# Kernel optimization log

Measured on AMD Instinct MI355X. Metric: run time of the kernel, lower is better.

Reference implementation:

```python
import jax, jax.numpy as jnp
import numpy as np

B, T, C = 4, 2048, 1024
NH = 16
HD = C // NH  # 64

def setup_inputs() -> dict:
    key = jax.random.key(0)
    k1, k2, k3 = jax.random.split(key, 3)
    x = jax.random.normal(k1, (B, T, C), dtype=jnp.float32)
    w_qkv = jax.random.normal(k2, (C, 3 * C), dtype=jnp.float32) * (1.0 / np.sqrt(C))
    w_out = jax.random.normal(k3, (C, C), dtype=jnp.float32) * (1.0 / np.sqrt(C))
    b_out = jnp.zeros((C,), dtype=jnp.float32)
    return {"x": x, "w_qkv": w_qkv, "w_out": w_out, "b_out": b_out}

def reference(x, w_qkv, w_out, b_out):
    b, t, c = x.shape
    nh, hd = NH, c // NH
    qkv = x @ w_qkv                      # [b, t, 3c]
    q, k, v = jnp.split(qkv, 3, axis=-1)
    # [b, t, c] -> [b, nh, t, hd]
    def heads(z):
        return z.reshape(b, t, nh, hd).transpose(0, 2, 1, 3)
    q, k, v = heads(q), heads(k), heads(v)
    scale = 1.0 / jnp.sqrt(jnp.asarray(hd, dtype=x.dtype))
    scores = jnp.einsum('bhqd,bhkd->bhqk', q, k) * scale  # [b, nh, t, t]
    causal = jnp.tril(jnp.ones((t, t), dtype=bool))
    scores = jnp.where(causal, scores, jnp.asarray(-jnp.inf, dtype=scores.dtype))
    attn = jax.nn.softmax(scores, axis=-1)
    ctx = jnp.einsum('bhqk,bhkd->bhqd', attn, v)           # [b, nh, t, hd]
    ctx = ctx.transpose(0, 2, 1, 3).reshape(b, t, c)
    return ctx @ w_out + b_out
```

## Files before the change

### kernel.cpp

```cpp
#include <hip/hip_runtime.h>
#include <cmath>


typedef __bf16 bf16x4 __attribute__((ext_vector_type(4)));
typedef __bf16 bf16x8 __attribute__((ext_vector_type(8)));
typedef float  f32x4  __attribute__((ext_vector_type(4)));
typedef float  f32x16 __attribute__((ext_vector_type(16)));

__device__ __forceinline__ void gload_lds16(const __bf16* g, __bf16* l) {
    __builtin_amdgcn_global_load_lds(
        (const __attribute__((address_space(1))) void*)g,
        (__attribute__((address_space(3))) void*)l,
        16, 0, 0);
}

__device__ __forceinline__ unsigned packbf(float a, float b) {
    union { __bf16 h[2]; unsigned u; } t;
    t.h[0] = (__bf16)a; t.h[1] = (__bf16)b;
    return t.u;
}

__device__ __forceinline__ void permswap(unsigned& a, unsigned& b) {
    asm volatile("v_permlane32_swap_b32 %0, %1" : "+v"(a), "+v"(b));
}

#define BAR()  __builtin_amdgcn_s_barrier()
#define VM2()  { asm volatile("s_waitcnt vmcnt(2)" ::: "memory"); \
                 __builtin_amdgcn_sched_barrier(0); }

__global__ __launch_bounds__(256) void cast_bf16(const float* __restrict__ in,
                                                 __bf16* __restrict__ out, int n4) {
    int i = blockIdx.x * 256 + threadIdx.x;
    if (i >= n4) return;
    float4 f = *(const float4*)(in + (size_t)i * 4);
    bf16x4 o;
    o[0] = (__bf16)f.x; o[1] = (__bf16)f.y; o[2] = (__bf16)f.z; o[3] = (__bf16)f.w;
    *(bf16x4*)(out + (size_t)i * 4) = o;
}

__global__ __launch_bounds__(256) void transpose_cast(const float* __restrict__ W,
                                                      __bf16* __restrict__ WT,
                                                      int K, int N,
                                                      int nScaleLim, float scale) {
    __shared__ float tile[32][33];
    const int n0 = blockIdx.x * 32, k0 = blockIdx.y * 32;
    const int tx = threadIdx.x & 31, ty = threadIdx.x >> 5;
    #pragma unroll
    for (int i = 0; i < 4; ++i)
        tile[ty + 8 * i][tx] = W[(size_t)(k0 + ty + 8 * i) * N + n0 + tx];
    __syncthreads();
    #pragma unroll
    for (int i = 0; i < 4; ++i) {
        const int n = n0 + ty + 8 * i;
        float v = tile[tx][ty + 8 * i];
        if (n < nScaleLim) v *= scale;
        WT[(size_t)n * K + k0 + tx] = (__bf16)v;
    }
}

template <typename OutT, bool BIAS, bool VOUT>
__global__ __launch_bounds__(512) void gemm256(const __bf16* __restrict__ A,
                                               const __bf16* __restrict__ BT,
                                               OutT* __restrict__ Cc,
                                               const float* __restrict__ bias,
                                               __bf16* __restrict__ Vt,
                                               int M, int N, int K) {
    __shared__ __attribute__((aligned(16))) char lds[98304];
    const int tid = threadIdx.x, lane = tid & 63, w = tid >> 6;
    const int wr = w >> 1, wc = w & 1, cc = lane & 15, gg = lane >> 4;

    const int cpx = gridDim.x >> 3;
    const int swz = ((int)blockIdx.x & 7) * cpx + ((int)blockIdx.x >> 3);
    const int nbx = N >> 7;
    const int rowBase = (swz / nbx) << 8;
    const int colBase = (swz % nbx) << 7;
    const int NT = K >> 6;

    const int sChunk = (lane & 7) ^ (((lane >> 5) & 1) << 1);
    const int rsub   = lane >> 3;

    auto stA = [&](int t, int h) {
        const int buf = t & 1, k0 = (t % NT) * 64;
        #pragma unroll
        for (int l = 0; l < 2; ++l) {
            int idx   = l * 8 + w;
            int rbase = h * 128 + idx * 8;
            gload_lds16(A + (size_t)(rowBase + rbase + rsub) * K + k0 + sChunk * 8,
                        (__bf16*)(lds + buf * 32768 + rbase * 128 + lane * 16));
        }
    };
    auto stB = [&](int t) {
        const int buf = t & 1, k0 = (t % NT) * 64;
        #pragma unroll
        for (int l = 0; l < 2; ++l) {
            int idx   = l * 8 + w;
            int rbase = idx * 8;
            gload_lds16(BT + (size_t)(colBase + rbase + rsub) * K + k0 + sChunk * 8,
                        (__bf16*)(lds + 65536 + buf * 16384 + rbase * 128 + lane * 16));
        }
    };

    f32x4 acc[4][4];
    #pragma unroll
    for (int i = 0; i < 4; ++i)
        #pragma unroll
        for (int j = 0; j < 4; ++j) acc[i][j] = f32x4{0.f, 0.f, 0.f, 0.f};
    bf16x8 afr[4], bfr[8];

    auto rdA = [&](int buf, int mh) {
        const char* base = lds + buf * 32768;
        #pragma unroll
        for (int i = 0; i < 2; ++i)
            #pragma unroll
            for (int kk = 0; kk < 2; ++kk) {
                int r  = wr * 64 + mh * 32 + i * 16 + cc;
                int cb = (kk * 64 + gg * 16) ^ (((cc >> 2) & 1) << 5);
                afr[i * 2 + kk] = *(const bf16x8*)(base + r * 128 + cb);
            }
    };
    auto rdB = [&](int buf) {
        const char* base = lds + 65536 + buf * 16384;
        #pragma unroll
        for (int j = 0; j < 4; ++j)
            #pragma unroll
            for (int kk = 0; kk < 2; ++kk) {
                int r  = wc * 64 + j * 16 + cc;
                int cb = (kk * 64 + gg * 16) ^ (((cc >> 2) & 1) << 5);
                bfr[j * 2 + kk] = *(const bf16x8*)(base + r * 128 + cb);
            }
    };

#define QMFMA(MH, NH)                                                        \
    _Pragma("unroll") for (int i = 0; i < 2; ++i)                            \
    _Pragma("unroll") for (int j = 0; j < 2; ++j)                            \
    _Pragma("unroll") for (int kk = 0; kk < 2; ++kk)                         \
        acc[(MH)*2 + i][(NH)*2 + j] = __builtin_amdgcn_mfma_f32_16x16x32_bf16( \
            afr[i*2 + kk], bfr[((NH)*2 + j)*2 + kk], acc[(MH)*2 + i][(NH)*2 + j], 0, 0, 0);

    stA(0, 0); stB(0); stA(0, 1); stB(1);
    VM2(); BAR();

    for (int t = 0; t < NT; ++t) {
        const int buf = t & 1;
        rdA(buf, 0); rdB(buf);
        stA(t + 1, 0);
        BAR();
        __builtin_amdgcn_s_setprio(1); QMFMA(0, 0); __builtin_amdgcn_s_setprio(0);
        BAR();
        stA(t + 1, 1);
        BAR();
        __builtin_amdgcn_s_setprio(1); QMFMA(0, 1); __builtin_amdgcn_s_setprio(0);
        BAR();
        rdA(buf, 1);
        stB(t + 2);
        BAR();
        __builtin_amdgcn_s_setprio(1); QMFMA(1, 0); __builtin_amdgcn_s_setprio(0);
        BAR();
        BAR();
        __builtin_amdgcn_s_setprio(1); QMFMA(1, 1); __builtin_amdgcn_s_setprio(0);
        VM2(); BAR();
    }
#undef QMFMA

    #pragma unroll
    for (int i = 0; i < 4; ++i)
        #pragma unroll
        for (int j = 0; j < 4; ++j) {
            const int col = colBase + wc * 64 + j * 16 + cc;
            #pragma unroll
            for (int rr = 0; rr < 4; ++rr) {
                const int row = rowBase + wr * 64 + i * 16 + gg * 4 + rr;
                float v = acc[i][j][rr];
                if (BIAS) v += bias[col];
                Cc[(size_t)row * N + col] = (OutT)v;
            }
            if (VOUT && col >= 2048) {
                const int bh16 = ((rowBase >> 11) << 4) + ((col - 2048) >> 6);
                const int d    = (col - 2048) & 63;
                const int t0   = (rowBase & 2047) + wr * 64 + i * 16 + gg * 4;
                union { bf16x4 v4; uint2 u; } pk;
                #pragma unroll
                for (int rr = 0; rr < 4; ++rr) pk.v4[rr] = (__bf16)acc[i][j][rr];
                *(uint2*)(Vt + ((size_t)bh16 * 64 + d) * 2048 + t0) = pk.u;
            }
        }
}

__global__ __launch_bounds__(256) void flash_attn_mfma(const __bf16* __restrict__ qkv,
                                                       const __bf16* __restrict__ Vt,
                                                       __bf16* __restrict__ ctx) {
    constexpr int T = 2048, C = 1024, HD = 64;
    constexpr int R3C = 3 * C;

    const int tid  = threadIdx.x;
    const int lane = tid & 63;
    const int w    = tid >> 6;
    const int q5   = lane & 31;
    const int half = lane >> 5;

    const int bh   = blockIdx.x;
    const int y    = blockIdx.y;
    const int qtA  = 15 - y;
    const int qtB  = y;
    const int b    = bh >> 4;
    const int h    = bh & 15;
    const int srowA = qtA * 128 + w * 32;
    const int srowB = qtB * 128 + w * 32;
    const int ktmaxA = qtA * 128 + 64;
    const int ktmaxB = qtB * 128 + 64;

    __shared__ __attribute__((aligned(16))) __bf16 KsL[2][64][64];
    __shared__ __attribute__((aligned(16))) __bf16 VsL[2][64][64];

    const __bf16* QrowA = qkv + (size_t)(b * T + srowA + q5) * R3C + h * HD;
    const __bf16* QrowB = qkv + (size_t)(b * T + srowB + q5) * R3C + h * HD;
    bf16x8 QbA[4], QbB[4];
    #pragma unroll
    for (int ks = 0; ks < 4; ++ks) {
        QbA[ks] = *(const bf16x8*)(QrowA + ks * 16 + half * 8);
        QbB[ks] = *(const bf16x8*)(QrowB + ks * 16 + half * 8);
    }

    f32x16 OA[2], OB[2];
    #pragma unroll
    for (int mb = 0; mb < 2; ++mb)
        #pragma unroll
        for (int r = 0; r < 16; ++r) { OA[mb][r] = 0.f; OB[mb][r] = 0.f; }
    float lsumA = 0.f, lsumB = 0.f;

    const __bf16* Kb  = qkv + (size_t)(b * T) * R3C + C + h * HD;
    const __bf16* Vtb = Vt + (size_t)bh * 64 * T;

    auto stage = [&](int bufi, int kt) {
        #pragma unroll
        for (int i = 0; i < 2; ++i) {
            int idx = tid + 256 * i;
            int kr  = idx >> 3;
            int c8  = idx & 7;
            int cs  = c8 ^ (kr & 7);
            gload_lds16(Kb + (size_t)(kt + kr) * R3C + cs * 8,
                        &KsL[bufi][kr][c8 * 8]);
        }
        #pragma unroll
        for (int i = 0; i < 2; ++i) {
            int idx = tid + 256 * i;
            int d   = idx >> 3;
            int k8  = idx & 7;
            int ks_ = k8 ^ (d & 7);
            gload_lds16(Vtb + (size_t)d * T + kt + ks_ * 8,
                        &VsL[bufi][d][k8 * 8]);
        }
    };

    stage(0, 0);
    __syncthreads();

    for (int kt = 0; kt <= ktmaxA; kt += 64) {
        const int cur = (kt >> 6) & 1;
        if (kt + 64 <= ktmaxA) stage(cur ^ 1, kt + 64);

        const char* kbase = (const char*)KsL[cur];
        const char* vbase = (const char*)VsL[cur];

        auto subtile = [&](int sub, const bf16x8* Qb, int srow, f32x16* O, float& lsum) {
            f32x16 S;
            #pragma unroll
            for (int r = 0; r < 16; ++r) S[r] = 0.f;
            const int krow = sub * 32 + q5;
            const int kxor = (krow & 7) << 4;
            #pragma unroll
            for (int ks = 0; ks < 4; ++ks) {
                bf16x8 kb = *(const bf16x8*)(kbase + krow * 128 +
                                             (((ks * 16 + half * 8) * 2) ^ kxor));
                S = __builtin_amdgcn_mfma_f32_32x32x16_bf16(kb, Qb[ks], S, 0, 0, 0);
            }
            if (kt + sub * 32 + 31 > srow) {
                #pragma unroll
                for (int r = 0; r < 16; ++r) {
                    int key = kt + sub * 32 + (r & 3) + 8 * (r >> 2) + 4 * half;
                    if (key > srow + q5) S[r] = -1e30f;
                }
            }
            float p[16];
            #pragma unroll
            for (int r = 0; r < 16; ++r) p[r] = exp2f(S[r]);
            {
                float a0 = (p[0] + p[1]) + (p[2] + p[3]);
                float a1 = (p[4] + p[5]) + (p[6] + p[7]);
                float a2 = (p[8] + p[9]) + (p[10] + p[11]);
                float a3 = (p[12] + p[13]) + (p[14] + p[15]);
                lsum += (a0 + a1) + (a2 + a3);
            }
            unsigned w0 = packbf(p[0],  p[1]);
            unsigned w1 = packbf(p[2],  p[3]);
            unsigned w2 = packbf(p[4],  p[5]);
            unsigned w3 = packbf(p[6],  p[7]);
            permswap(w0, w2);
            permswap(w1, w3);
            unsigned w4 = packbf(p[8],  p[9]);
            unsigned w5 = packbf(p[10], p[11]);
            unsigned w6 = packbf(p[12], p[13]);
            unsigned w7 = packbf(p[14], p[15]);
            permswap(w4, w6);
            permswap(w5, w7);
            union { unsigned u[4]; bf16x8 v; } pf0, pf1;
            pf0.u[0] = w0; pf0.u[1] = w1; pf0.u[2] = w2; pf0.u[3] = w3;
            pf1.u[0] = w4; pf1.u[1] = w5; pf1.u[2] = w6; pf1.u[3] = w7;
            const int vc = sub * 32 + half * 8;
            #pragma unroll
            for (int mb = 0; mb < 2; ++mb) {
                const int vrow = mb * 32 + q5;
                const int vxor = (vrow & 7) << 4;
                bf16x8 v0 = *(const bf16x8*)(vbase + vrow * 128 + ((vc * 2) ^ vxor));
                O[mb] = __builtin_amdgcn_mfma_f32_32x32x16_bf16(v0, pf0.v, O[mb], 0, 0, 0);
                bf16x8 v1 = *(const bf16x8*)(vbase + vrow * 128 + (((vc + 16) * 2) ^ vxor));
                O[mb] = __builtin_amdgcn_mfma_f32_32x32x16_bf16(v1, pf1.v, O[mb], 0, 0, 0);
            }
        };

        #pragma unroll
        for (int sub = 0; sub < 2; ++sub)
            subtile(sub, QbA, srowA, OA, lsumA);
        if (kt <= ktmaxB) {
            #pragma unroll
            for (int sub = 0; sub < 2; ++sub)
                subtile(sub, QbB, srowB, OB, lsumB);
        }

        __syncthreads();
    }

    const float invA = 1.f / (lsumA + __shfl_xor(lsumA, 32));
    const float invB = 1.f / (lsumB + __shfl_xor(lsumB, 32));

    __bf16* crowA = ctx + (size_t)(b * T + srowA + q5) * C + h * HD;
    __bf16* crowB = ctx + (size_t)(b * T + srowB + q5) * C + h * HD;
    #pragma unroll
    for (int mb = 0; mb < 2; ++mb)
        #pragma unroll
        for (int a = 0; a < 4; ++a) {
            union { bf16x4 v; uint2 u; } pA, pB;
            #pragma unroll
            for (int bq = 0; bq < 4; ++bq) {
                pA.v[bq] = (__bf16)(OA[mb][4 * a + bq] * invA);
                pB.v[bq] = (__bf16)(OB[mb][4 * a + bq] * invB);
            }
            *(uint2*)(crowA + mb * 32 + 8 * a + 4 * half) = pA.u;
            *(uint2*)(crowB + mb * 32 + 8 * a + 4 * half) = pB.u;
        }
}

extern "C" void kernel_launch(void* const* d_in, const int* in_sizes, int n_in,
                              void* d_out, int out_size, void* d_ws, size_t ws_size,
                              hipStream_t stream) {
    constexpr int B = 4, T = 2048, C = 1024;
    constexpr int M = B * T;
    constexpr float K1 = 0.125f * 1.44269504088896f;

    const float* x     = (const float*)d_in[0];
    const float* w_qkv = (const float*)d_in[1];
    const float* w_out = (const float*)d_in[2];
    const float* b_out = (const float*)d_in[3];
    float* out = (float*)d_out;

    char* ws = (char*)d_ws;
    __bf16* xb     = (__bf16*)(ws);
    __bf16* wqkvT  = (__bf16*)(ws + (16ull << 20));
    __bf16* woutT  = (__bf16*)(ws + (22ull << 20));
    __bf16* qkvb   = (__bf16*)(ws + (24ull << 20));
    __bf16* ctxb   = (__bf16*)(ws + (72ull << 20));
    __bf16* Vt     = (__bf16*)(ws + (88ull << 20));

    cast_bf16<<<(M * C / 4 + 255) / 256, 256, 0, stream>>>(x, xb, M * C / 4);
    transpose_cast<<<dim3(3 * C / 32, C / 32), 256, 0, stream>>>(
        w_qkv, wqkvT, C, 3 * C, 1024, K1);
    transpose_cast<<<dim3(C / 32, C / 32), 256, 0, stream>>>(
        w_out, woutT, C, C, 0, 1.0f);

    gemm256<__bf16, false, true><<<768, 512, 0, stream>>>(
        xb, wqkvT, qkvb, nullptr, Vt, M, 3 * C, C);

    flash_attn_mfma<<<dim3(B * 16, 8), 256, 0, stream>>>(qkvb, Vt, ctxb);

    gemm256<float, true, false><<<256, 512, 0, stream>>>(
        ctxb, woutT, out, b_out, nullptr, M, C, C);
}
```

Baseline: 273.4 us.

## Split paired causal query tiles into separate blocks with interleaved tile order

Each flash-attention block used to handle two query tiles (a long and a short one) so causal work was balanced and K/V tiles were shared between them. Now each block handles one query tile, the grid doubles to 16 tiles per head, and tiles are mapped in an interleaved order so long and short tiles are mixed across blocks. This lowers per-block registers (one accumulator set instead of two), which may raise occupancy, and gives more blocks to spread over CUs. The cost is that K/V tiles are loaded twice as often and per-block work becomes uneven again.

```diff
diff --git a/kernel.cpp b/kernel.cpp
--- a/kernel.cpp
+++ b/kernel.cpp
@@ -198,35 +198,33 @@
     const int q5   = lane & 31;
     const int half = lane >> 5;
 
-    const int bh   = blockIdx.x;
-    const int y    = blockIdx.y;
-    const int qtA  = 15 - y;
-    const int qtB  = y;
-    const int b    = bh >> 4;
-    const int h    = bh & 15;
-    const int srowA = qtA * 128 + w * 32;
-    const int srowB = qtB * 128 + w * 32;
-    const int ktmaxA = qtA * 128 + 64;
-    const int ktmaxB = qtB * 128 + 64;
+    const int bh = blockIdx.x;
+    const int y  = blockIdx.y;
+    const int rr_ = y >> 2, cc_ = y & 3;
+    const int qt  = (rr_ == 0) ? 2 * cc_
+                  : (rr_ == 1) ? 15 - 2 * cc_
+                  : (rr_ == 2) ? 2 * cc_ + 1
+                               : 14 - 2 * cc_;
+    const int b     = bh >> 4;
+    const int h     = bh & 15;
+    const int srow  = qt * 128 + w * 32;
+    const int ktmax = qt * 128 + 64;
 
     __shared__ __attribute__((aligned(16))) __bf16 KsL[2][64][64];
     __shared__ __attribute__((aligned(16))) __bf16 VsL[2][64][64];
 
-    const __bf16* QrowA = qkv + (size_t)(b * T + srowA + q5) * R3C + h * HD;
-    const __bf16* QrowB = qkv + (size_t)(b * T + srowB + q5) * R3C + h * HD;
-    bf16x8 QbA[4], QbB[4];
-    #pragma unroll
-    for (int ks = 0; ks < 4; ++ks) {
-        QbA[ks] = *(const bf16x8*)(QrowA + ks * 16 + half * 8);
-        QbB[ks] = *(const bf16x8*)(QrowB + ks * 16 + half * 8);
-    }
-
-    f32x16 OA[2], OB[2];
+    const __bf16* Qrow = qkv + (size_t)(b * T + srow + q5) * R3C + h * HD;
+    bf16x8 Qb[4];
+    #pragma unroll
+    for (int ks = 0; ks < 4; ++ks)
+        Qb[ks] = *(const bf16x8*)(Qrow + ks * 16 + half * 8);
+
+    f32x16 O[2];
     #pragma unroll
     for (int mb = 0; mb < 2; ++mb)
         #pragma unroll
-        for (int r = 0; r < 16; ++r) { OA[mb][r] = 0.f; OB[mb][r] = 0.f; }
-    float lsumA = 0.f, lsumB = 0.f;
+        for (int r = 0; r < 16; ++r) O[mb][r] = 0.f;
+    float lsum = 0.f;
 
     const __bf16* Kb  = qkv + (size_t)(b * T) * R3C + C + h * HD;
     const __bf16* Vtb = Vt + (size_t)bh * 64 * T;
@@ -255,14 +253,14 @@
     stage(0, 0);
     __syncthreads();
 
-    for (int kt = 0; kt <= ktmaxA; kt += 64) {
+    for (int kt = 0; kt <= ktmax; kt += 64) {
         const int cur = (kt >> 6) & 1;
-        if (kt + 64 <= ktmaxA) stage(cur ^ 1, kt + 64);
+        if (kt + 64 <= ktmax) stage(cur ^ 1, kt + 64);
 
         const char* kbase = (const char*)KsL[cur];
         const char* vbase = (const char*)VsL[cur];
 
-        auto subtile = [&](int sub, const bf16x8* Qb, int srow, f32x16* O, float& lsum) {
+        auto subtile = [&](int sub) {
             f32x16 S;
             #pragma unroll
             for (int r = 0; r < 16; ++r) S[r] = 0.f;
@@ -318,35 +316,24 @@
             }
         };
 
-        #pragma unroll
-        for (int sub = 0; sub < 2; ++sub)
-            subtile(sub, QbA, srowA, OA, lsumA);
-        if (kt <= ktmaxB) {
-            #pragma unroll
-            for (int sub = 0; sub < 2; ++sub)
-                subtile(sub, QbB, srowB, OB, lsumB);
-        }
+        subtile(0);
+        subtile(1);
 
         __syncthreads();
     }
 
-    const float invA = 1.f / (lsumA + __shfl_xor(lsumA, 32));
-    const float invB = 1.f / (lsumB + __shfl_xor(lsumB, 32));
-
-    __bf16* crowA = ctx + (size_t)(b * T + srowA + q5) * C + h * HD;
-    __bf16* crowB = ctx + (size_t)(b * T + srowB + q5) * C + h * HD;
+    const float inv = 1.f / (lsum + __shfl_xor(lsum, 32));
+
+    __bf16* crow = ctx + (size_t)(b * T + srow + q5) * C + h * HD;
     #pragma unroll
     for (int mb = 0; mb < 2; ++mb)
         #pragma unroll
         for (int a = 0; a < 4; ++a) {
-            union { bf16x4 v; uint2 u; } pA, pB;
-            #pragma unroll
-            for (int bq = 0; bq < 4; ++bq) {
-                pA.v[bq] = (__bf16)(OA[mb][4 * a + bq] * invA);
-                pB.v[bq] = (__bf16)(OB[mb][4 * a + bq] * invB);
-            }
-            *(uint2*)(crowA + mb * 32 + 8 * a + 4 * half) = pA.u;
-            *(uint2*)(crowB + mb * 32 + 8 * a + 4 * half) = pB.u;
+            union { bf16x4 v; uint2 u; } pk;
+            #pragma unroll
+            for (int bq = 0; bq < 4; ++bq)
+                pk.v[bq] = (__bf16)(O[mb][4 * a + bq] * inv);
+            *(uint2*)(crow + mb * 32 + 8 * a + 4 * half) = pk.u;
         }
 }
 
@@ -380,7 +367,7 @@
     gemm256<__bf16, false, true><<<768, 512, 0, stream>>>(
         xb, wqkvT, qkvb, nullptr, Vt, M, 3 * C, C);
 
-    flash_attn_mfma<<<dim3(B * 16, 8), 256, 0, stream>>>(qkvb, Vt, ctxb);
+    flash_attn_mfma<<<dim3(B * 16, 16), 256, 0, stream>>>(qkvb, Vt, ctxb);
 
     gemm256<float, true, false><<<256, 512, 0, stream>>>(
         ctxb, woutT, out, b_out, nullptr, M, C, C);
```

Result: slower. 283.7 us (+3.8%).
